# Performance work log

Measured on AMD Instinct MI355X. Metric: run time of the kernel, lower is better.

Reference implementation:

```python
import jax, jax.numpy as jnp
import numpy as np
from jax import lax

EPS = 1e-5


def _bn(h, g, b):
    # BatchNorm in training mode: batch statistics, biased variance.
    if h.ndim == 3:
        ax, shp = (0, 2), (1, -1, 1)
    else:
        ax, shp = (0,), (1, -1)
    m = h.mean(ax).reshape(shp)
    v = h.var(ax).reshape(shp)
    return (h - m) / jnp.sqrt(v + EPS) * g.reshape(shp) + b.reshape(shp)


def _conv1d(h, w, b, stride):
    y = lax.conv_general_dilated(h, w, (stride,), 'VALID',
                                 dimension_numbers=('NCH', 'OIH', 'NCH'))
    return y + b[None, :, None]


def setup_inputs() -> dict:
    key = jax.random.key(0)
    ks = jax.random.split(key, 16)
    N, L, C = 1024, 8064, 32
    L3, n_half = 27, 13
    s = 0.05
    inp = {
        'x': jax.random.normal(ks[0], (N, L), jnp.float32),
        'perm_idx': jax.random.randint(ks[1], (N, n_half), 0, L3, jnp.int32),
        'A': jax.random.uniform(ks[2], (N, N), jnp.float32),
        'conv1_w': jax.random.normal(ks[3], (C, 1, 13), jnp.float32) * s,
        'conv1_b': jnp.zeros((C,), jnp.float32),
        'conv2_w': jax.random.normal(ks[4], (C, C, 12), jnp.float32) * s,
        'conv2_b': jnp.zeros((C,), jnp.float32),
        'conv3_w': jax.random.normal(ks[5], (C, C, 24), jnp.float32) * s,
        'conv3_b': jnp.zeros((C,), jnp.float32),
        'bn1_g': jnp.ones((C,), jnp.float32), 'bn1_b': jnp.zeros((C,), jnp.float32),
        'bn2_g': jnp.ones((C,), jnp.float32), 'bn2_b': jnp.zeros((C,), jnp.float32),
        'bn3_g': jnp.ones((3 * C,), jnp.float32), 'bn3_b': jnp.zeros((3 * C,), jnp.float32),
        'bn4_g': jnp.ones((C,), jnp.float32), 'bn4_b': jnp.zeros((C,), jnp.float32),
        'fc1_w': jax.random.normal(ks[6], (C, 3 * C), jnp.float32) * s,
        'fc1_b': jnp.zeros((C,), jnp.float32),
        'gcn_w': jax.random.normal(ks[7], (C, 2 * C), jnp.float32) * s,
        'gcn_b': jnp.zeros((C,), jnp.float32),
    }
    return inp


def reference(x, perm_idx, A, conv1_w, conv1_b, conv2_w, conv2_b, conv3_w, conv3_b,
              bn1_g, bn1_b, bn2_g, bn2_b, bn3_g, bn3_b, bn4_g, bn4_b,
              fc1_w, fc1_b, gcn_w, gcn_b):
    h = _conv1d(x[:, None, :], conv1_w, conv1_b, 1)       # [N,32,8052]
    h = _bn(jax.nn.relu(h), bn1_g, bn1_b)
    h = _conv1d(h, conv2_w, conv2_b, 12)                  # [N,32,671]
    h = _bn(jax.nn.relu(h), bn2_g, bn2_b)
    h = _conv1d(h, conv3_w, conv3_b, 24)                  # [N,32,27]
    # per-sample random half subsample -> explicit gather of selected columns
    sel = jnp.take_along_axis(h, perm_idx[:, None, :], axis=2)  # [N,32,13]
    mu = sel.mean(axis=2)
    sd = jnp.std(sel, axis=2, ddof=1)   # torch.std is unbiased
    mx = sel.max(axis=2)
    f = jnp.concatenate([mu, sd, mx], axis=1)             # [N,96]
    f = _bn(f, bn3_g, bn3_b)
    f = jax.nn.relu(f @ fc1_w.T + fc1_b)                  # [N,32]
    f = _bn(f, bn4_g, bn4_b)
    # gcn(order=1, support=[A]): nconv 'vl,vw->wl' == A.T @ f
    x1 = A.T @ f                                          # [N,32]
    hcat = jnp.concatenate([f, x1], axis=1)               # [N,64]
    return hcat @ gcn_w.T + gcn_b                         # [N,32]
```

## Files before the change

kernel.cpp:

```cpp
#include <hip/hip_runtime.h>

#define EPS 1e-5f
#define NB 1024
#define LX 8064
#define C  32
#define L1 8052
#define L2 671
#define L3 27
#define NH 13

typedef short bf16x8 __attribute__((ext_vector_type(8)));
typedef float f32x4  __attribute__((ext_vector_type(4)));

#define WS_BN1P 0
#define WS_BN2P 1024
#define WS_BN3P 3072
#define WS_BN4P 6144
#define WS_ZEROF 7168
#define WS_SC3  7168
#define WS_SH3  7264
#define WS_SC4  7360
#define WS_SH4  7392
#define WS_B2F  7424
#define WS_B3F  7456
#define WS_W2B  7488
#define WS_W3F  19776
#define WS_FRAW 44352
#define WS_FC   142656
#define WS_H2   175424
#define WS_TOTALF (WS_H2 + (size_t)NB * C * L2)

static __device__ __forceinline__ unsigned short f2bf(float x) {
    union { float f; unsigned u; } v; v.f = x;
    unsigned r = (v.u + 0x7FFFu + ((v.u >> 16) & 1u)) >> 16;
    return (unsigned short)r;
}
static __device__ __forceinline__ float bf2f(unsigned short h) {
    union { unsigned u; float f; } v; v.u = ((unsigned)h) << 16;
    return v.f;
}

__global__ __launch_bounds__(256) void k1_conv1_stats(
    const float* __restrict__ x, const float* __restrict__ w1,
    const float* __restrict__ b1, float* __restrict__ ws)
{
    __shared__ __align__(16) float xs[LX];
    __shared__ float red[2][C];
    const int n = blockIdx.x, t = threadIdx.x;
    for (int i = 4 * t; i < LX; i += 1024)
        *(float4*)&xs[i] = *(const float4*)&x[n * LX + i];
    if (t < 2 * C) ((float*)red)[t] = 0.f;
    __syncthreads();
    const int c = t & 31, g = t >> 5;
    float w[13];
#pragma unroll
    for (int k = 0; k < 13; ++k) w[k] = w1[c * 13 + k];
    const float bias = b1[c];
    float s = 0.f, ss = 0.f;
    for (int m = g; m < 2013; m += 8) {
        const int p = 4 * m;
        float4 a0 = *(const float4*)&xs[p];
        float4 a1 = *(const float4*)&xs[p + 4];
        float4 a2 = *(const float4*)&xs[p + 8];
        float4 a3 = *(const float4*)&xs[p + 12];
        float xv[16] = {a0.x,a0.y,a0.z,a0.w, a1.x,a1.y,a1.z,a1.w,
                        a2.x,a2.y,a2.z,a2.w, a3.x,a3.y,a3.z,a3.w};
#pragma unroll
        for (int u = 0; u < 4; ++u) {
            float acc = bias;
#pragma unroll
            for (int k = 0; k < 13; ++k) acc = fmaf(w[k], xv[u + k], acc);
            acc = fmaxf(acc, 0.f);
            s += acc; ss = fmaf(acc, acc, ss);
        }
    }
    atomicAdd(&red[0][c], s);
    atomicAdd(&red[1][c], ss);
    __syncthreads();
    if (t < C) {
        const int bkt = n & 15;
        atomicAdd(&ws[WS_BN1P + bkt * 64 + t], red[0][t]);
        atomicAdd(&ws[WS_BN1P + bkt * 64 + 32 + t], red[1][t]);
    }
}

__global__ __launch_bounds__(256) void k2_fold_bn1(
    const float* __restrict__ w2, const float* __restrict__ b2,
    const float* __restrict__ g1, const float* __restrict__ bb1,
    float* __restrict__ ws)
{
    __shared__ float sc[C], sh[C];
    const int t = threadIdx.x;
    if (t < C) {
        float s = 0.f, q = 0.f;
        for (int b = 0; b < 16; ++b) {
            s += ws[WS_BN1P + b * 64 + t];
            q += ws[WS_BN1P + b * 64 + 32 + t];
        }
        const float cnt = (float)NB * (float)L1;
        const float m = s / cnt;
        const float v = q / cnt - m * m;
        const float scale = g1[t] / sqrtf(v + EPS);
        sc[t] = scale;
        sh[t] = bb1[t] - m * scale;
    }
    __syncthreads();
    unsigned short* __restrict__ w2b = (unsigned short*)(ws + WS_W2B);
    for (int idx = t; idx < C * C * 12; idx += 256) {
        const float wf = w2[idx] * sc[(idx / 12) & 31];
        const unsigned short hi = f2bf(wf);
        const unsigned short lo = f2bf(wf - bf2f(hi));
        w2b[idx] = hi;
        w2b[C * C * 12 + idx] = lo;
    }
    if (t < C) {
        float acc = b2[t];
        for (int i = 0; i < C; ++i) {
            float wsum = 0.f;
            const float* wr = w2 + t * 384 + i * 12;
#pragma unroll
            for (int k = 0; k < 12; ++k) wsum += wr[k];
            acc = fmaf(wsum, sh[i], acc);
        }
        ws[WS_B2F + t] = acc;
    }
}

#define TL 32
#define PT (12 * TL)
#define AS 392

__global__ __launch_bounds__(256) void k3_conv12(
    const float* __restrict__ x, const float* __restrict__ w1,
    const float* __restrict__ b1, float* __restrict__ ws)
{
    __shared__ __align__(16) unsigned short h1hi[TL][AS];
    __shared__ __align__(16) unsigned short h1lo[TL][AS];
    __shared__ __align__(16) float xs[PT + 12];
    __shared__ float red[2][C];
    const int tile = blockIdx.x, n = blockIdx.y, t = threadIdx.x;
    const int l0 = tile * TL;
    const int nl = min(TL, L2 - l0);
    const int np = nl * 12;
    const int p0 = l0 * 12;
    for (int i = 4 * t; i < np + 12; i += 1024)
        *(float4*)&xs[i] = *(const float4*)&x[n * LX + p0 + i];
    if (nl < TL) {
        for (int idx = t; idx < AS; idx += 256) {
            h1hi[TL - 1][idx] = 0;
            h1lo[TL - 1][idx] = 0;
        }
    }
    if (t < 2 * C) ((float*)red)[t] = 0.f;
    __syncthreads();
    {
        const int c = t & 31, g = t >> 5;
        float w[13];
#pragma unroll
        for (int k = 0; k < 13; ++k) w[k] = w1[c * 13 + k];
        const float bias = b1[c];
        for (int m = g; 4 * m < np; m += 8) {
            const int p = 4 * m;
            float4 a0 = *(const float4*)&xs[p];
            float4 a1 = *(const float4*)&xs[p + 4];
            float4 a2 = *(const float4*)&xs[p + 8];
            float4 a3 = *(const float4*)&xs[p + 12];
            float xv[16] = {a0.x,a0.y,a0.z,a0.w, a1.x,a1.y,a1.z,a1.w,
                            a2.x,a2.y,a2.z,a2.w, a3.x,a3.y,a3.z,a3.w};
            ushort4 hi4, lo4;
            float h[4];
#pragma unroll
            for (int u = 0; u < 4; ++u) {
                float acc = bias;
#pragma unroll
                for (int k = 0; k < 13; ++k) acc = fmaf(w[k], xv[u + k], acc);
                h[u] = fmaxf(acc, 0.f);
            }
            hi4.x = f2bf(h[0]); hi4.y = f2bf(h[1]);
            hi4.z = f2bf(h[2]); hi4.w = f2bf(h[3]);
            lo4.x = f2bf(h[0] - bf2f(hi4.x));
            lo4.y = f2bf(h[1] - bf2f(hi4.y));
            lo4.z = f2bf(h[2] - bf2f(hi4.z));
            lo4.w = f2bf(h[3] - bf2f(hi4.w));
            const int l = p / 12, kk0 = p - l * 12;
            const int off = c * 12 + kk0;
            *(ushort4*)&h1hi[l][off] = hi4;
            *(ushort4*)&h1lo[l][off] = lo4;
        }
    }
    __syncthreads();
    {
        const int wv = t >> 6, lane = t & 63;
        const int m15 = lane & 15, kg = lane >> 4;
        const int lh = (wv >> 1) << 4, oh = (wv & 1) << 4;
        const int o = oh + m15;
        const unsigned short* __restrict__ w2b = (const unsigned short*)(ws + WS_W2B);
        const unsigned short* __restrict__ wh = w2b + o * 384 + kg * 8;
        const unsigned short* __restrict__ wl = wh + C * C * 12;
        const unsigned short* __restrict__ ah = &h1hi[lh + m15][kg * 8];
        const unsigned short* __restrict__ al = &h1lo[lh + m15][kg * 8];
        const float bias = ws[WS_B2F + o];
        f32x4 acc = {bias, bias, bias, bias};
#pragma unroll
        for (int kk = 0; kk < 12; ++kk) {
            const bf16x8 ahi = *(const bf16x8*)(ah + kk * 32);
            const bf16x8 alo = *(const bf16x8*)(al + kk * 32);
            const bf16x8 bhi = *(const bf16x8*)(wh + kk * 32);
            const bf16x8 blo = *(const bf16x8*)(wl + kk * 32);
            acc = __builtin_amdgcn_mfma_f32_16x16x32_bf16(ahi, bhi, acc, 0, 0, 0);
            acc = __builtin_amdgcn_mfma_f32_16x16x32_bf16(ahi, blo, acc, 0, 0, 0);
            acc = __builtin_amdgcn_mfma_f32_16x16x32_bf16(alo, bhi, acc, 0, 0, 0);
        }
        const int lbase = lh + kg * 4;
        float* __restrict__ hp = ws + WS_H2 + ((size_t)(n * C + o)) * L2 + l0 + lbase;
        float s = 0.f, ss = 0.f;
#pragma unroll
        for (int r = 0; r < 4; ++r) {
            const float v = fmaxf(acc[r], 0.f);
            if (lbase + r < nl) {
                hp[r] = v;
                s += v; ss = fmaf(v, v, ss);
            }
        }
        s  += __shfl_xor(s, 16);  s  += __shfl_xor(s, 32);
        ss += __shfl_xor(ss, 16); ss += __shfl_xor(ss, 32);
        if (kg == 0) {
            atomicAdd(&red[0][o], s);
            atomicAdd(&red[1][o], ss);
        }
    }
    __syncthreads();
    if (t < C) {
        const int bkt = (tile + 21 * n) & 31;
        atomicAdd(&ws[WS_BN2P + bkt * 64 + t], red[0][t]);
        atomicAdd(&ws[WS_BN2P + bkt * 64 + 32 + t], red[1][t]);
    }
}

__global__ __launch_bounds__(256) void k4_fold_bn2(
    const float* __restrict__ w3, const float* __restrict__ b3,
    const float* __restrict__ g2, const float* __restrict__ bb2,
    float* __restrict__ ws)
{
    __shared__ float sc[C], sh[C];
    const int t = threadIdx.x;
    if (t < C) {
        float s = 0.f, q = 0.f;
        for (int b = 0; b < 32; ++b) {
            s += ws[WS_BN2P + b * 64 + t];
            q += ws[WS_BN2P + b * 64 + 32 + t];
        }
        const float cnt = (float)NB * (float)L2;
        const float m = s / cnt;
        const float v = q / cnt - m * m;
        const float scale = g2[t] / sqrtf(v + EPS);
        sc[t] = scale;
        sh[t] = bb2[t] - m * scale;
    }
    __syncthreads();
    for (int idx = t; idx < C * C * 24; idx += 256)
        ws[WS_W3F + idx] = w3[idx] * sc[(idx / 24) & 31];
    if (t < C) {
        float acc = b3[t];
        for (int i = 0; i < C; ++i) {
            float wsum = 0.f;
            const float* wr = w3 + t * 768 + i * 24;
#pragma unroll
            for (int k = 0; k < 24; ++k) wsum += wr[k];
            acc = fmaf(wsum, sh[i], acc);
        }
        ws[WS_B3F + t] = acc;
    }
}

__global__ __launch_bounds__(256) void k5_conv3_pool(
    const int* __restrict__ perm, float* __restrict__ ws)
{
    __shared__ __align__(16) float row[648];
    __shared__ __align__(16) float wsl[C * 24];
    __shared__ float h3s[C][L3];
    const int n = blockIdx.x, t = threadIdx.x;
    const float* __restrict__ h2n = ws + WS_H2 + (size_t)n * (C * L2);
    float acc[4] = {0.f, 0.f, 0.f, 0.f};
    for (int i = 0; i < C; ++i) {
        __syncthreads();
        for (int idx = t; idx < 648; idx += 256) row[idx] = h2n[i * L2 + idx];
        for (int idx = t; idx < C * 24; idx += 256)
            wsl[idx] = ws[WS_W3F + (idx / 24) * 768 + i * 24 + (idx % 24)];
        __syncthreads();
#pragma unroll
        for (int jj = 0; jj < 4; ++jj) {
            const int idx = t + jj * 256;
            if (idx < C * L3) {
                const int c = idx / L3, tt = idx % L3;
                float a = acc[jj];
                const float* wr = &wsl[c * 24];
                const float* rr = &row[24 * tt];
#pragma unroll
                for (int k = 0; k < 24; ++k) a = fmaf(wr[k], rr[k], a);
                acc[jj] = a;
            }
        }
    }
    __syncthreads();
#pragma unroll
    for (int jj = 0; jj < 4; ++jj) {
        const int idx = t + jj * 256;
        if (idx < C * L3) {
            const int c = idx / L3, tt = idx % L3;
            h3s[c][tt] = acc[jj] + ws[WS_B3F + c];
        }
    }
    __syncthreads();
    if (t < C) {
        int pidx[NH];
#pragma unroll
        for (int j = 0; j < NH; ++j) pidx[j] = perm[n * NH + j];
        float vals[NH];
#pragma unroll
        for (int j = 0; j < NH; ++j) vals[j] = h3s[t][pidx[j]];
        float s = 0.f;
#pragma unroll
        for (int j = 0; j < NH; ++j) s += vals[j];
        const float mu = s * (1.f / 13.f);
        float va = 0.f;
#pragma unroll
        for (int j = 0; j < NH; ++j) { const float d = vals[j] - mu; va = fmaf(d, d, va); }
        const float sd = sqrtf(va * (1.f / 12.f));
        float mx = vals[0];
#pragma unroll
        for (int j = 1; j < NH; ++j) mx = fmaxf(mx, vals[j]);
        float* fr = ws + WS_FRAW + n * 96;
        fr[t] = mu; fr[32 + t] = sd; fr[64 + t] = mx;
        const int bkt = n & 15;
        float* bp = ws + WS_BN3P + bkt * 192;
        atomicAdd(&bp[t], mu);
        atomicAdd(&bp[32 + t], sd);
        atomicAdd(&bp[64 + t], mx);
        atomicAdd(&bp[96 + t], mu * mu);
        atomicAdd(&bp[128 + t], sd * sd);
        atomicAdd(&bp[160 + t], mx * mx);
    }
}

__global__ __launch_bounds__(128) void k5b_bn3(
    const float* __restrict__ g3, const float* __restrict__ bb3,
    float* __restrict__ ws)
{
    const int t = threadIdx.x;
    if (t < 96) {
        float s = 0.f, q = 0.f;
        for (int b = 0; b < 16; ++b) {
            s += ws[WS_BN3P + b * 192 + t];
            q += ws[WS_BN3P + b * 192 + 96 + t];
        }
        const float m = s / 1024.f;
        const float v = q / 1024.f - m * m;
        const float scale = g3[t] / sqrtf(v + EPS);
        ws[WS_SC3 + t] = scale;
        ws[WS_SH3 + t] = bb3[t] - m * scale;
    }
}

__global__ __launch_bounds__(256) void k6_fc1(
    const float* __restrict__ fw, const float* __restrict__ fb,
    float* __restrict__ ws)
{
    __shared__ float wl[C][97];
    __shared__ __align__(16) float fbn[64][96];
    __shared__ float red[2][C];
    const int b = blockIdx.x, t = threadIdx.x;
    const int n0 = b * 64;
    for (int idx = t; idx < C * 96; idx += 256) wl[idx / 96][idx % 96] = fw[idx];
    if (t < 2 * C) ((float*)red)[t] = 0.f;
    for (int idx = t; idx < 64 * 96; idx += 256) {
        const int r = idx / 96, j = idx % 96;
        fbn[r][j] = fmaf(ws[WS_FRAW + (n0 + r) * 96 + j], ws[WS_SC3 + j], ws[WS_SH3 + j]);
    }
    __syncthreads();
    const int o = t & 31, rg = t >> 5;
    const float bo = fb[o];
    float s = 0.f, ss = 0.f;
    for (int mI = 0; mI < 8; ++mI) {
        const int r = rg + 8 * mI;
        float a = bo;
#pragma unroll
        for (int j = 0; j < 96; ++j) a = fmaf(wl[o][j], fbn[r][j], a);
        a = fmaxf(a, 0.f);
        ws[WS_FC + (n0 + r) * C + o] = a;
        s += a; ss = fmaf(a, a, ss);
    }
    atomicAdd(&red[0][o], s);
    atomicAdd(&red[1][o], ss);
    __syncthreads();
    if (t < C) {
        ws[WS_BN4P + b * 64 + t] = red[0][t];
        ws[WS_BN4P + b * 64 + 32 + t] = red[1][t];
    }
}

__global__ __launch_bounds__(64) void k6b_bn4(
    const float* __restrict__ g4, const float* __restrict__ bb4,
    float* __restrict__ ws)
{
    const int t = threadIdx.x;
    if (t < C) {
        float s = 0.f, q = 0.f;
        for (int b = 0; b < 16; ++b) {
            s += ws[WS_BN4P + b * 64 + t];
            q += ws[WS_BN4P + b * 64 + 32 + t];
        }
        const float m = s / 1024.f;
        const float v = q / 1024.f - m * m;
        const float scale = g4[t] / sqrtf(v + EPS);
        ws[WS_SC4 + t] = scale;
        ws[WS_SH4 + t] = bb4[t] - m * scale;
    }
}

__global__ __launch_bounds__(256) void k7_gcn(
    const float* __restrict__ A, const float* __restrict__ gw,
    const float* __restrict__ gb, const float* __restrict__ ws,
    float* __restrict__ out)
{
    __shared__ float As[8][64];
    __shared__ float fs[8][C];
    __shared__ float gws[C][65];
    __shared__ float f4s[64][C];
    __shared__ float x1s[64][C];
    const int t = threadIdx.x;
    const int w0 = blockIdx.x * 64;
    const int c = t & 31, wg = t >> 5;
    const float scC = ws[WS_SC4 + c], shC = ws[WS_SH4 + c];
    for (int idx = t; idx < 2048; idx += 256) gws[idx >> 6][idx & 63] = gw[idx];
    for (int idx = t; idx < 2048; idx += 256) {
        const int r = idx >> 5;
        f4s[r][c] = fmaf(ws[WS_FC + (w0 + r) * C + c], scC, shC);
    }
    float acc[8] = {0, 0, 0, 0, 0, 0, 0, 0};
    for (int v0 = 0; v0 < NB; v0 += 8) {
        __syncthreads();
        {
            const int vv = t >> 6, wl = t & 63;
            As[vv][wl]     = A[(size_t)(v0 + vv) * NB + w0 + wl];
            As[vv + 4][wl] = A[(size_t)(v0 + vv + 4) * NB + w0 + wl];
        }
        {
            const int vv = t >> 5;
            fs[vv][c] = fmaf(ws[WS_FC + (v0 + vv) * C + c], scC, shC);
        }
        __syncthreads();
#pragma unroll
        for (int vv = 0; vv < 8; ++vv) {
            const float fv = fs[vv][c];
#pragma unroll
            for (int j = 0; j < 8; ++j)
                acc[j] = fmaf(As[vv][wg + 8 * j], fv, acc[j]);
        }
    }
    __syncthreads();
#pragma unroll
    for (int j = 0; j < 8; ++j) x1s[wg + 8 * j][c] = acc[j];
    __syncthreads();
    const float gbv = gb[c];
#pragma unroll
    for (int j = 0; j < 8; ++j) {
        const int wl = wg + 8 * j;
        float a = gbv;
#pragma unroll
        for (int cc = 0; cc < C; ++cc) {
            a = fmaf(gws[c][cc],      f4s[wl][cc], a);
            a = fmaf(gws[c][32 + cc], x1s[wl][cc], a);
        }
        out[(w0 + wl) * C + c] = a;
    }
}

extern "C" void kernel_launch(void* const* d_in, const int* in_sizes, int n_in,
                              void* d_out, int out_size, void* d_ws, size_t ws_size,
                              hipStream_t stream)
{
    (void)in_sizes; (void)n_in; (void)out_size;
    const float* x    = (const float*)d_in[0];
    const int*   perm = (const int*)  d_in[1];
    const float* A    = (const float*)d_in[2];
    const float* c1w  = (const float*)d_in[3];
    const float* c1b  = (const float*)d_in[4];
    const float* c2w  = (const float*)d_in[5];
    const float* c2b  = (const float*)d_in[6];
    const float* c3w  = (const float*)d_in[7];
    const float* c3b  = (const float*)d_in[8];
    const float* g1   = (const float*)d_in[9];
    const float* bb1  = (const float*)d_in[10];
    const float* g2   = (const float*)d_in[11];
    const float* bb2  = (const float*)d_in[12];
    const float* g3   = (const float*)d_in[13];
    const float* bb3  = (const float*)d_in[14];
    const float* g4   = (const float*)d_in[15];
    const float* bb4  = (const float*)d_in[16];
    const float* fw   = (const float*)d_in[17];
    const float* fb   = (const float*)d_in[18];
    const float* gw   = (const float*)d_in[19];
    const float* gb   = (const float*)d_in[20];
    float* ws  = (float*)d_ws;
    float* out = (float*)d_out;

    if (ws_size < WS_TOTALF * sizeof(float)) return;

    hipMemsetAsync(d_ws, 0, WS_ZEROF * sizeof(float), stream);
    k1_conv1_stats<<<dim3(NB), dim3(256), 0, stream>>>(x, c1w, c1b, ws);
    k2_fold_bn1  <<<dim3(1),  dim3(256), 0, stream>>>(c2w, c2b, g1, bb1, ws);
    k3_conv12    <<<dim3(21, NB), dim3(256), 0, stream>>>(x, c1w, c1b, ws);
    k4_fold_bn2  <<<dim3(1),  dim3(256), 0, stream>>>(c3w, c3b, g2, bb2, ws);
    k5_conv3_pool<<<dim3(NB), dim3(256), 0, stream>>>(perm, ws);
    k5b_bn3      <<<dim3(1),  dim3(128), 0, stream>>>(g3, bb3, ws);
    k6_fc1       <<<dim3(16), dim3(256), 0, stream>>>(fw, fb, ws);
    k6b_bn4      <<<dim3(1),  dim3(64),  0, stream>>>(g4, bb4, ws);
    k7_gcn       <<<dim3(16), dim3(256), 0, stream>>>(A, gw, gb, ws, out);
}
```

Baseline: 737.7 us.

## Halve conv1+conv2 tile length and split MFMA K-loop across waves

The fused conv1/conv2 kernel now processes 16 output positions per block instead of 32, doubling the grid to 42×1024 blocks and halving shared memory per block. To keep all four waves busy with the smaller tile, the 12-step MFMA reduction is split in half across wave pairs, with partial sums combined through shared memory before bias, ReLU, store and stats. This aims for higher occupancy and more blocks in flight, at the cost of an extra barrier, a shared-memory reduction, and recomputing the conv1 halo and doubling BN atomics per output.

Measured after the change: 738.6 us. Within noise of the previous version (+0.1%).

```diff
diff --git a/kernel.cpp b/kernel.cpp
--- a/kernel.cpp
+++ b/kernel.cpp
@@ -126,7 +126,7 @@
     }
 }
 
-#define TL 32
+#define TL 16
 #define PT (12 * TL)
 #define AS 392
 
@@ -136,7 +136,8 @@
 {
     __shared__ __align__(16) unsigned short h1hi[TL][AS];
     __shared__ __align__(16) unsigned short h1lo[TL][AS];
-    __shared__ __align__(16) float xs[PT + 12];
+    __shared__ __align__(16) float xs[PT + 16];
+    __shared__ float red4[2][16][16];
     __shared__ float red[2][C];
     const int tile = blockIdx.x, n = blockIdx.y, t = threadIdx.x;
     const int l0 = tile * TL;
@@ -192,17 +193,17 @@
     {
         const int wv = t >> 6, lane = t & 63;
         const int m15 = lane & 15, kg = lane >> 4;
-        const int lh = (wv >> 1) << 4, oh = (wv & 1) << 4;
+        const int oh = (wv & 1) << 4;
+        const int kb = (wv >> 1) * 6;
         const int o = oh + m15;
         const unsigned short* __restrict__ w2b = (const unsigned short*)(ws + WS_W2B);
-        const unsigned short* __restrict__ wh = w2b + o * 384 + kg * 8;
+        const unsigned short* __restrict__ wh = w2b + o * 384 + kb * 32 + kg * 8;
         const unsigned short* __restrict__ wl = wh + C * C * 12;
-        const unsigned short* __restrict__ ah = &h1hi[lh + m15][kg * 8];
-        const unsigned short* __restrict__ al = &h1lo[lh + m15][kg * 8];
-        const float bias = ws[WS_B2F + o];
-        f32x4 acc = {bias, bias, bias, bias};
-#pragma unroll
-        for (int kk = 0; kk < 12; ++kk) {
+        const unsigned short* __restrict__ ah = &h1hi[m15][kb * 32 + kg * 8];
+        const unsigned short* __restrict__ al = &h1lo[m15][kb * 32 + kg * 8];
+        f32x4 acc = {0.f, 0.f, 0.f, 0.f};
+#pragma unroll
+        for (int kk = 0; kk < 6; ++kk) {
             const bf16x8 ahi = *(const bf16x8*)(ah + kk * 32);
             const bf16x8 alo = *(const bf16x8*)(al + kk * 32);
             const bf16x8 bhi = *(const bf16x8*)(wh + kk * 32);
@@ -211,27 +212,36 @@
             acc = __builtin_amdgcn_mfma_f32_16x16x32_bf16(ahi, blo, acc, 0, 0, 0);
             acc = __builtin_amdgcn_mfma_f32_16x16x32_bf16(alo, bhi, acc, 0, 0, 0);
         }
-        const int lbase = lh + kg * 4;
-        float* __restrict__ hp = ws + WS_H2 + ((size_t)(n * C + o)) * L2 + l0 + lbase;
-        float s = 0.f, ss = 0.f;
-#pragma unroll
-        for (int r = 0; r < 4; ++r) {
-            const float v = fmaxf(acc[r], 0.f);
-            if (lbase + r < nl) {
-                hp[r] = v;
-                s += v; ss = fmaf(v, v, ss);
+        if (wv >= 2) {
+#pragma unroll
+            for (int r = 0; r < 4; ++r) red4[wv & 1][kg * 4 + r][m15] = acc[r];
+        }
+        __syncthreads();
+        if (wv < 2) {
+            const float bias = ws[WS_B2F + o];
+            float* __restrict__ hp = ws + WS_H2 + ((size_t)(n * C + o)) * L2 + l0;
+            float s = 0.f, ss = 0.f;
+#pragma unroll
+            for (int r = 0; r < 4; ++r) {
+                const int l = kg * 4 + r;
+                float v = acc[r] + red4[wv & 1][l][m15] + bias;
+                v = fmaxf(v, 0.f);
+                if (l < nl) {
+                    hp[l] = v;
+                    s += v; ss = fmaf(v, v, ss);
+                }
             }
-        }
-        s  += __shfl_xor(s, 16);  s  += __shfl_xor(s, 32);
-        ss += __shfl_xor(ss, 16); ss += __shfl_xor(ss, 32);
-        if (kg == 0) {
-            atomicAdd(&red[0][o], s);
-            atomicAdd(&red[1][o], ss);
-        }
-    }
-    __syncthreads();
-    if (t < C) {
-        const int bkt = (tile + 21 * n) & 31;
+            s  += __shfl_xor(s, 16);  s  += __shfl_xor(s, 32);
+            ss += __shfl_xor(ss, 16); ss += __shfl_xor(ss, 32);
+            if (kg == 0) {
+                atomicAdd(&red[0][o], s);
+                atomicAdd(&red[1][o], ss);
+            }
+        }
+    }
+    __syncthreads();
+    if (t < C) {
+        const int bkt = (tile + 13 * n) & 31;
         atomicAdd(&ws[WS_BN2P + bkt * 64 + t], red[0][t]);
         atomicAdd(&ws[WS_BN2P + bkt * 64 + 32 + t], red[1][t]);
     }
@@ -510,7 +520,7 @@
     hipMemsetAsync(d_ws, 0, WS_ZEROF * sizeof(float), stream);
     k1_conv1_stats<<<dim3(NB), dim3(256), 0, stream>>>(x, c1w, c1b, ws);
     k2_fold_bn1  <<<dim3(1),  dim3(256), 0, stream>>>(c2w, c2b, g1, bb1, ws);
-    k3_conv12    <<<dim3(21, NB), dim3(256), 0, stream>>>(x, c1w, c1b, ws);
+    k3_conv12    <<<dim3(42, NB), dim3(256), 0, stream>>>(x, c1w, c1b, ws);
     k4_fold_bn2  <<<dim3(1),  dim3(256), 0, stream>>>(c3w, c3b, g2, bb2, ws);
     k5_conv3_pool<<<dim3(NB), dim3(256), 0, stream>>>(perm, ws);
     k5b_bn3      <<<dim3(1),  dim3(128), 0, stream>>>(g3, bb3, ws);
```
